# Kernel tuning notes

Hardware: AMD Instinct MI355X
Metric: run time of the kernel (lower is better)

The kernel has to match this reference:

```python
import jax, jax.numpy as jnp
import numpy as np

NUM_HEADS = 12
NUM_PATCHES = 196


def _make_relative_distance_index(num_patches=NUM_PATCHES):
    size = int(np.sqrt(num_patches))  # 14
    coords = np.stack(np.meshgrid(np.arange(size), np.arange(size), indexing='ij'))  # [2,14,14]
    flat = coords.reshape(2, -1)  # [2,196]
    rel = flat[:, None, :] - flat[:, :, None]  # [2,196,196]
    rel = rel.transpose(1, 2, 0).astype(np.int64)  # [196,196,2]
    rel[:, :, 0] += size - 1
    rel[:, :, 1] += size - 1
    rel[:, :, 0] *= 2 * size - 1
    idx = rel.sum(-1) + 1  # shift for cls slot at table row 0
    full = np.zeros((num_patches + 1, num_patches + 1), dtype=np.int64)
    full[1:, 1:] = idx
    return full


def setup_inputs() -> dict:
    key = jax.random.key(0)
    k1, k2, k3, k4, k5 = jax.random.split(key, 5)
    B, N, C = 64, NUM_PATCHES + 1, 768
    table_size = (2 * int(np.sqrt(NUM_PATCHES)) - 1) ** 2 + 1  # 730
    x = jax.random.normal(k1, (B, N, C), dtype=jnp.float32)
    table = jax.random.normal(k2, (table_size, NUM_HEADS), dtype=jnp.float32) * 0.02
    w_qkv = jax.random.normal(k3, (3 * C, C), dtype=jnp.float32) * 0.02
    w_proj = jax.random.normal(k4, (C, C), dtype=jnp.float32) * 0.02
    b_proj = jax.random.normal(k5, (C,), dtype=jnp.float32) * 0.02
    rel_index = jnp.asarray(_make_relative_distance_index())
    return {"x": x, "table": table, "w_qkv": w_qkv, "w_proj": w_proj,
            "b_proj": b_proj, "rel_index": rel_index}


def reference(x, table, w_qkv, w_proj, b_proj, rel_index):
    B, N, C = x.shape
    H = NUM_HEADS
    hd = C // H
    scale = hd ** -0.5
    # qkv projection: [B,N,3C] -> [3,B,H,N,hd]
    qkv = (x @ w_qkv.T).reshape(B, N, 3, H, hd).transpose(2, 0, 3, 1, 4)
    q, k, v = qkv[0], qkv[1], qkv[2]
    # gathered relative position bias: [N,N,H] -> [H,N,N]
    bias = table[rel_index].transpose(2, 0, 1)
    scores = jnp.einsum('bhnd,bhmd->bhnm', q, k) * scale + bias[None]
    attn = jax.nn.softmax(scores, axis=-1)
    out = jnp.einsum('bhnm,bhmd->bhnd', attn, v)
    out = out.transpose(0, 2, 1, 3).reshape(B, N, C)
    return out @ w_proj.T + b_proj
```

## Files before the change

### kernel.cpp

```cpp
#include <hip/hip_runtime.h>


#define NB   64
#define NN   197
#define NC   768
#define NH   12
#define HD   64
#define MM   (NB*NN)
#define MR   12672
#define NP   208
#define VS   212
#define SZQ  ((size_t)NB * NH * NN * HD)
#define CVTQ ((MM + 2304 + 768) * 192)
#define BIASN (NH * 13 * 13 * 256)

typedef unsigned short ushort_t;
typedef __attribute__((ext_vector_type(8))) short short8;
typedef __attribute__((ext_vector_type(4))) float f32x4;
union U128 { uint4 u; short8 s; };

__device__ __forceinline__ unsigned bf16_rne(float f) {
    unsigned u = __float_as_uint(f);
    return (u + 0x7fffu + ((u >> 16) & 1u)) >> 16;
}

__device__ __forceinline__ void gld16(unsigned short* lds, const unsigned short* g) {
    __builtin_amdgcn_global_load_lds(
        (const __attribute__((address_space(1))) void*)g,
        (__attribute__((address_space(3))) void*)lds, 16, 0, 0);
}

__global__ __launch_bounds__(256) void prepare(
    const float* __restrict__ x, const float* __restrict__ w_qkv,
    const float* __restrict__ w_proj, const float* __restrict__ table,
    const int* __restrict__ rel_index,
    ushort_t* __restrict__ xh, ushort_t* __restrict__ wh,
    ushort_t* __restrict__ wp, float* __restrict__ biasP)
{
    int idx = blockIdx.x * 256 + threadIdx.x;
    if (idx < CVTQ) {
        int r = idx / 192;
        int c = (idx - r * 192) * 4;
        const float* src;
        ushort_t* dsth;
        if (r < MM) {
            src = x + (size_t)r * NC; dsth = xh + (size_t)r * NC + c;
        } else if (r < MM + 2304) {
            int rr = r - MM;
            src = w_qkv + (size_t)rr * NC; dsth = wh + (size_t)rr * NC + c;
        } else {
            int rr = r - MM - 2304;
            src = w_proj + (size_t)rr * NC; dsth = wp + (size_t)rr * NC + c;
        }
        float4 f = *(const float4*)(src + c);
        ushort4 hv = { (ushort_t)bf16_rne(f.x), (ushort_t)bf16_rne(f.y),
                       (ushort_t)bf16_rne(f.z), (ushort_t)bf16_rne(f.w) };
        *(ushort4*)dsth = hv;
    } else {
        int i = idx - CVTQ;
        if (i < BIASN) {
            int r = i & 3, l15 = (i >> 2) & 15, quad = (i >> 6) & 3;
            int t = i >> 8;
            int kt = t % 13; int t2 = t / 13;
            int qt = t2 % 13; int h = t2 / 13;
            int n = qt * 16 + quad * 4 + r;
            int m = kt * 16 + l15;
            float v = -1e30f;
            if (n < NN && m < NN) v = table[rel_index[n * NN + m] * NH + h];
            biasP[i] = v;
        }
    }
}

__device__ __forceinline__ void gemm_mainloop(
    const ushort_t* __restrict__ A2, int sA,
    const ushort_t* __restrict__ B2, int sB,
    int m0, int n0, int kiters, ushort_t* Abuf, ushort_t* Bbuf, f32x4 acc[4][8])
{
    const int tid = threadIdx.x;
    const int w = tid >> 6, lane = tid & 63;
    const int wm = w & 1, wn = w >> 1;
    const int lr = lane >> 3, lc = lane & 7;
    const int gch = lc ^ lr;

    const ushort_t* Ag = A2 + (size_t)(m0 + w * 32 + lr) * sA + gch * 8;
    const ushort_t* Bg = B2 + (size_t)(n0 + w * 64 + lr) * sB + gch * 8;
    ushort_t* Al = Abuf + (w * 32) * 64;
    ushort_t* Bl = Bbuf + (w * 64) * 64;

    int aoff[4], boff[8];
    const int quad = lane >> 4, l15 = lane & 15;
    #pragma unroll
    for (int t = 0; t < 4; t++) {
        int ra = wm * 64 + t * 16 + l15;
        aoff[t] = ra * 64 + ((quad ^ (ra & 7)) << 3);
    }
    #pragma unroll
    for (int j = 0; j < 8; j++) {
        int rb = wn * 128 + j * 16 + l15;
        boff[j] = rb * 64 + ((quad ^ (rb & 7)) << 3);
    }

    for (int ks = 0; ks < kiters; ks++) {
        __syncthreads();
        #pragma unroll
        for (int it = 0; it < 4; it++)
            gld16(Al + it * 8 * 64, Ag + (size_t)it * 8 * sA);
        #pragma unroll
        for (int it = 0; it < 8; it++)
            gld16(Bl + it * 8 * 64, Bg + (size_t)it * 8 * sB);
        __syncthreads();
        #pragma unroll
        for (int k0 = 0; k0 < 2; k0++) {
            U128 af[4], bf[8];
            #pragma unroll
            for (int t = 0; t < 4; t++)
                af[t].u = *(const uint4*)&Abuf[aoff[t] ^ (k0 << 5)];
            #pragma unroll
            for (int j = 0; j < 8; j++)
                bf[j].u = *(const uint4*)&Bbuf[boff[j] ^ (k0 << 5)];
            #pragma unroll
            for (int i = 0; i < 4; i++)
                #pragma unroll
                for (int j = 0; j < 8; j++)
                    acc[i][j] = __builtin_amdgcn_mfma_f32_16x16x32_bf16(
                        af[i].s, bf[j].s, acc[i][j], 0, 0, 0);
        }
        Ag += 64; Bg += 64;
    }
}

__device__ __forceinline__ int xcd_remap(int bid, int nwg) {
    int q8 = nwg >> 3, r8 = nwg & 7;
    int xcd = bid & 7, loc = bid >> 3;
    return (xcd < r8 ? xcd * (q8 + 1) : r8 * (q8 + 1) + (xcd - r8) * q8) + loc;
}

__global__ __launch_bounds__(256, 2) void gemm_qkv_mfma(
    const ushort_t* __restrict__ A2, const ushort_t* __restrict__ B2,
    ushort_t* __restrict__ qbf, ushort_t* __restrict__ kbf,
    ushort_t* __restrict__ vbf)
{
    __shared__ ushort_t Abuf[128 * 64];
    __shared__ ushort_t Bbuf[256 * 64];
    f32x4 acc[4][8];
    f32x4 z = {0.f, 0.f, 0.f, 0.f};
    #pragma unroll
    for (int i = 0; i < 4; i++)
        #pragma unroll
        for (int j = 0; j < 8; j++) acc[i][j] = z;

    int f = xcd_remap(blockIdx.x, 891);
    int mt_ = f / 9, nt_ = f - mt_ * 9;
    const int m0 = mt_ * 128, n0 = nt_ * 256;
    gemm_mainloop(A2, NC, B2, NC, m0, n0, 12, Abuf, Bbuf, acc);

    __syncthreads();

    const int tid = threadIdx.x;
    const int w = tid >> 6, lane = tid & 63;
    const int wm = w & 1, wn = w >> 1;
    const int quad = lane >> 4, l15 = lane & 15;

    ushort_t* Sw = Abuf + w * 1152;
    const int orow = lane >> 2;
    const int dch = (lane & 3) << 3;
    #pragma unroll
    for (int mt = 0; mt < 4; mt++) {
        int m = m0 + wm * 64 + mt * 16 + orow;
        int b_ = m / NN, n_ = m - b_ * NN;
        bool mv = (m < MM);
        #pragma unroll
        for (int g = 0; g < 2; g++) {
            int cg = n0 + wn * 128 + g * 64;
            int tq = cg / NC;
            int wi = cg - tq * NC;
            int hh = wi >> 6;
            ushort_t* dst = (tq == 0) ? qbf : (tq == 1) ? kbf : vbf;
            float scale = (tq == 0) ? 0.125f : 1.0f;
            #pragma unroll
            for (int nt = 0; nt < 4; nt++)
                #pragma unroll
                for (int r = 0; r < 4; r++)
                    Sw[(quad * 4 + r) * 72 + nt * 16 + l15] =
                        (ushort_t)bf16_rne(acc[mt][g * 4 + nt][r] * scale);
            if (mv) {
                size_t rb = ((size_t)(b_ * NH + hh) * NN + n_) * HD;
                uint4 v0 = *(const uint4*)&Sw[orow * 72 + dch];
                uint4 v1 = *(const uint4*)&Sw[orow * 72 + dch + 32];
                *(uint4*)&dst[rb + dch] = v0;
                *(uint4*)&dst[rb + dch + 32] = v1;
            }
        }
    }
}

__global__ __launch_bounds__(256, 2) void gemm_proj_mfma(
    const ushort_t* __restrict__ A2, const ushort_t* __restrict__ B2,
    const float* __restrict__ bias, float* __restrict__ out)
{
    __shared__ ushort_t Abuf[128 * 64];
    __shared__ ushort_t Bbuf[256 * 64];
    f32x4 acc[4][8];
    f32x4 z = {0.f, 0.f, 0.f, 0.f};
    #pragma unroll
    for (int i = 0; i < 4; i++)
        #pragma unroll
        for (int j = 0; j < 8; j++) acc[i][j] = z;

    int f = xcd_remap(blockIdx.x, 297);
    int mt_ = f / 3, nt_ = f - mt_ * 3;
    const int m0 = mt_ * 128, n0 = nt_ * 256;
    gemm_mainloop(A2, NC, B2, NC, m0, n0, 12, Abuf, Bbuf, acc);

    const int tid = threadIdx.x;
    const int w = tid >> 6, lane = tid & 63;
    const int wm = w & 1, wn = w >> 1;
    const int quad = lane >> 4, l15 = lane & 15;
    #pragma unroll
    for (int nt = 0; nt < 8; nt++) {
        int col = n0 + wn * 128 + nt * 16 + l15;
        float bi = bias[col];
        #pragma unroll
        for (int mt = 0; mt < 4; mt++) {
            #pragma unroll
            for (int r = 0; r < 4; r++) {
                int m = m0 + wm * 64 + mt * 16 + quad * 4 + r;
                if (m < MM)
                    out[(size_t)m * NC + col] = acc[mt][nt][r] + bi;
            }
        }
    }
}

__global__ __launch_bounds__(256, 2) void attn_mfma(
    const ushort_t* __restrict__ qbf, const ushort_t* __restrict__ kbf,
    const ushort_t* __restrict__ vbf, const float* __restrict__ biasP,
    ushort_t* __restrict__ ab)
{
    __shared__ ushort_t Kl[NP * 64];
    __shared__ ushort_t Vt[64 * VS];
    __shared__ ushort_t Pl[4][16 * VS];

    const int bh = blockIdx.x;
    const int b = bh / NH, h = bh % NH;
    const int tid = threadIdx.x;
    const int w = tid >> 6, lane = tid & 63;
    const int quad = lane >> 4, l15 = lane & 15;
    const size_t base = (size_t)bh * (NN * HD);
    const ushort_t* kg = kbf + base;
    const ushort_t* vg = vbf + base;
    const ushort_t* qg = qbf + base;

    for (int idx = tid; idx < NP * 8; idx += 256) {
        int row = idx >> 3, ch = idx & 7;
        int srow = (row < NN) ? row : (NN - 1);
        uint4 val = *(const uint4*)(kg + (size_t)srow * HD + ch * 8);
        *(uint4*)&Kl[row * 64 + ((ch ^ (row & 7)) << 3)] = val;
    }

    ushort_t* Vstage = &Pl[0][0];
    for (int idx = tid; idx < NP * 8; idx += 256) {
        int row = idx >> 3, ch = idx & 7;
        uint4 val = {0u, 0u, 0u, 0u};
        if (row < NN) val = *(const uint4*)(vg + (size_t)row * HD + ch * 8);
        *(uint4*)&Vstage[row * HD + ch * 8] = val;
    }
    __syncthreads();
    for (int task = tid; task < 64 * 26; task += 256) {
        int d = task & 63, kc = task >> 6;
        ushort_t tmp[8];
        #pragma unroll
        for (int j = 0; j < 8; j++)
            tmp[j] = Vstage[(kc * 8 + j) * HD + d];
        uint4 u;
        u.x = (unsigned)tmp[0] | ((unsigned)tmp[1] << 16);
        u.y = (unsigned)tmp[2] | ((unsigned)tmp[3] << 16);
        u.z = (unsigned)tmp[4] | ((unsigned)tmp[5] << 16);
        u.w = (unsigned)tmp[6] | ((unsigned)tmp[7] << 16);
        *(uint4*)&Vt[d * VS + kc * 8] = u;
    }
    __syncthreads();

    const int ksl = (quad ^ (l15 & 7)) << 3;
    ushort_t* P = Pl[w];

    #pragma unroll
    for (int rep = 0; rep < 2; rep++) {
        const int qtA = w + rep * 8;
        const int qtB = qtA + 4;
        const bool hasB = (qtB <= 12);

        const int q0A = qtA * 16;
        int qrA = q0A + l15; if (qrA > NN - 1) qrA = NN - 1;
        U128 qA0, qA1;
        qA0.u = *(const uint4*)(qg + (size_t)qrA * HD + quad * 8);
        qA1.u = *(const uint4*)(qg + (size_t)qrA * HD + 32 + quad * 8);
        f32x4 SA[13];
        const float* bpA = biasP + ((size_t)(h * 13 + qtA) * 13) * 256 + (quad << 6) + (l15 << 2);
        #pragma unroll
        for (int kt = 0; kt < 13; kt++) {
            float4 bv = *(const float4*)(bpA + kt * 256);
            SA[kt][0] = bv.x; SA[kt][1] = bv.y; SA[kt][2] = bv.z; SA[kt][3] = bv.w;
        }

        const int q0B = qtB * 16;
        U128 qB0, qB1;
        f32x4 SB[13];
        if (hasB) {
            int qrB = q0B + l15; if (qrB > NN - 1) qrB = NN - 1;
            qB0.u = *(const uint4*)(qg + (size_t)qrB * HD + quad * 8);
            qB1.u = *(const uint4*)(qg + (size_t)qrB * HD + 32 + quad * 8);
            const float* bpB = biasP + ((size_t)(h * 13 + qtB) * 13) * 256 + (quad << 6) + (l15 << 2);
            #pragma unroll
            for (int kt = 0; kt < 13; kt++) {
                float4 bv = *(const float4*)(bpB + kt * 256);
                SB[kt][0] = bv.x; SB[kt][1] = bv.y; SB[kt][2] = bv.z; SB[kt][3] = bv.w;
            }
        }

        if (hasB) {
            #pragma unroll
            for (int kt = 0; kt < 13; kt++) {
                int ro = (kt * 16 + l15) * 64 + ksl;
                U128 k0, k1;
                k0.u = *(const uint4*)&Kl[ro];
                k1.u = *(const uint4*)&Kl[ro ^ 32];
                SA[kt] = __builtin_amdgcn_mfma_f32_16x16x32_bf16(qA0.s, k0.s, SA[kt], 0, 0, 0);
                SB[kt] = __builtin_amdgcn_mfma_f32_16x16x32_bf16(qB0.s, k0.s, SB[kt], 0, 0, 0);
                SA[kt] = __builtin_amdgcn_mfma_f32_16x16x32_bf16(qA1.s, k1.s, SA[kt], 0, 0, 0);
                SB[kt] = __builtin_amdgcn_mfma_f32_16x16x32_bf16(qB1.s, k1.s, SB[kt], 0, 0, 0);
            }
        } else {
            #pragma unroll
            for (int kt = 0; kt < 13; kt++) {
                int ro = (kt * 16 + l15) * 64 + ksl;
                U128 k0, k1;
                k0.u = *(const uint4*)&Kl[ro];
                k1.u = *(const uint4*)&Kl[ro ^ 32];
                SA[kt] = __builtin_amdgcn_mfma_f32_16x16x32_bf16(qA0.s, k0.s, SA[kt], 0, 0, 0);
                SA[kt] = __builtin_amdgcn_mfma_f32_16x16x32_bf16(qA1.s, k1.s, SA[kt], 0, 0, 0);
            }
        }

        #pragma unroll
        for (int r = 0; r < 4; r++) {
            float mx = SA[0][r];
            #pragma unroll
            for (int kt = 1; kt < 13; kt++) mx = fmaxf(mx, SA[kt][r]);
            mx = fmaxf(mx, __shfl_xor(mx, 1));
            mx = fmaxf(mx, __shfl_xor(mx, 2));
            mx = fmaxf(mx, __shfl_xor(mx, 4));
            mx = fmaxf(mx, __shfl_xor(mx, 8));
            float sum = 0.f;
            #pragma unroll
            for (int kt = 0; kt < 13; kt++) {
                float e = __expf(SA[kt][r] - mx);
                SA[kt][r] = e;
                sum += e;
            }
            sum += __shfl_xor(sum, 1);
            sum += __shfl_xor(sum, 2);
            sum += __shfl_xor(sum, 4);
            sum += __shfl_xor(sum, 8);
            float inv = 1.0f / sum;
            int prow = quad * 4 + r;
            #pragma unroll
            for (int kt = 0; kt < 13; kt++)
                P[prow * VS + kt * 16 + l15] = (ushort_t)bf16_rne(SA[kt][r] * inv);
        }

        f32x4 OA[4];
        f32x4 z4 = {0.f, 0.f, 0.f, 0.f};
        #pragma unroll
        for (int dt = 0; dt < 4; dt++) OA[dt] = z4;
        #pragma unroll
        for (int ks = 0; ks < 7; ks++) {
            int pc = ks * 32 + quad * 8;
            bool vld = (pc < NP);
            int pcc = vld ? pc : 0;
            U128 pf;
            pf.u = *(const uint4*)&P[l15 * VS + pcc];
            if (!vld) { pf.u.x = 0u; pf.u.y = 0u; pf.u.z = 0u; pf.u.w = 0u; }
            #pragma unroll
            for (int dt = 0; dt < 4; dt++) {
                U128 vf;
                vf.u = *(const uint4*)&Vt[(dt * 16 + l15) * VS + pcc];
                OA[dt] = __builtin_amdgcn_mfma_f32_16x16x32_bf16(pf.s, vf.s, OA[dt], 0, 0, 0);
            }
        }

        f32x4 OB[4];
        if (hasB) {
            #pragma unroll
            for (int r = 0; r < 4; r++) {
                float mx = SB[0][r];
                #pragma unroll
                for (int kt = 1; kt < 13; kt++) mx = fmaxf(mx, SB[kt][r]);
                mx = fmaxf(mx, __shfl_xor(mx, 1));
                mx = fmaxf(mx, __shfl_xor(mx, 2));
                mx = fmaxf(mx, __shfl_xor(mx, 4));
                mx = fmaxf(mx, __shfl_xor(mx, 8));
                float sum = 0.f;
                #pragma unroll
                for (int kt = 0; kt < 13; kt++) {
                    float e = __expf(SB[kt][r] - mx);
                    SB[kt][r] = e;
                    sum += e;
                }
                sum += __shfl_xor(sum, 1);
                sum += __shfl_xor(sum, 2);
                sum += __shfl_xor(sum, 4);
                sum += __shfl_xor(sum, 8);
                float inv = 1.0f / sum;
                int prow = quad * 4 + r;
                #pragma unroll
                for (int kt = 0; kt < 13; kt++)
                    P[prow * VS + kt * 16 + l15] = (ushort_t)bf16_rne(SB[kt][r] * inv);
            }
            #pragma unroll
            for (int dt = 0; dt < 4; dt++) OB[dt] = z4;
            #pragma unroll
            for (int ks = 0; ks < 7; ks++) {
                int pc = ks * 32 + quad * 8;
                bool vld = (pc < NP);
                int pcc = vld ? pc : 0;
                U128 pf;
                pf.u = *(const uint4*)&P[l15 * VS + pcc];
                if (!vld) { pf.u.x = 0u; pf.u.y = 0u; pf.u.z = 0u; pf.u.w = 0u; }
                #pragma unroll
                for (int dt = 0; dt < 4; dt++) {
                    U128 vf;
                    vf.u = *(const uint4*)&Vt[(dt * 16 + l15) * VS + pcc];
                    OB[dt] = __builtin_amdgcn_mfma_f32_16x16x32_bf16(pf.s, vf.s, OB[dt], 0, 0, 0);
                }
            }
        }

        {
            float* Osh = (float*)&Pl[w][0];
            #pragma unroll
            for (int dt = 0; dt < 4; dt++)
                #pragma unroll
                for (int r = 0; r < 4; r++)
                    Osh[(quad * 4 + r) * 68 + dt * 16 + l15] = OA[dt][r];
            int orow = lane >> 2;
            int d0 = (lane & 3) << 4;
            int q = q0A + orow;
            if (q < NN) {
                unsigned hiw[8];
                #pragma unroll
                for (int k4 = 0; k4 < 4; k4++) {
                    float4 f = *(const float4*)&Osh[orow * 68 + d0 + k4 * 4];
                    unsigned h0 = bf16_rne(f.x), h1 = bf16_rne(f.y);
                    unsigned h2 = bf16_rne(f.z), h3 = bf16_rne(f.w);
                    hiw[k4 * 2]     = h0 | (h1 << 16);
                    hiw[k4 * 2 + 1] = h2 | (h3 << 16);
                }
                size_t baseo = ((size_t)b * NN + q) * NC + h * HD + d0;
                uint4 hA = {hiw[0], hiw[1], hiw[2], hiw[3]};
                uint4 hB = {hiw[4], hiw[5], hiw[6], hiw[7]};
                *(uint4*)&ab[baseo] = hA;
                *(uint4*)&ab[baseo + 8] = hB;
            }
        }
        if (hasB) {
            float* Osh = (float*)&Pl[w][0];
            #pragma unroll
            for (int dt = 0; dt < 4; dt++)
                #pragma unroll
                for (int r = 0; r < 4; r++)
                    Osh[(quad * 4 + r) * 68 + dt * 16 + l15] = OB[dt][r];
            int orow = lane >> 2;
            int d0 = (lane & 3) << 4;
            int q = q0B + orow;
            if (q < NN) {
                unsigned hiw[8];
                #pragma unroll
                for (int k4 = 0; k4 < 4; k4++) {
                    float4 f = *(const float4*)&Osh[orow * 68 + d0 + k4 * 4];
                    unsigned h0 = bf16_rne(f.x), h1 = bf16_rne(f.y);
                    unsigned h2 = bf16_rne(f.z), h3 = bf16_rne(f.w);
                    hiw[k4 * 2]     = h0 | (h1 << 16);
                    hiw[k4 * 2 + 1] = h2 | (h3 << 16);
                }
                size_t baseo = ((size_t)b * NN + q) * NC + h * HD + d0;
                uint4 hA = {hiw[0], hiw[1], hiw[2], hiw[3]};
                uint4 hB = {hiw[4], hiw[5], hiw[6], hiw[7]};
                *(uint4*)&ab[baseo] = hA;
                *(uint4*)&ab[baseo + 8] = hB;
            }
        }
    }
}

extern "C" void kernel_launch(void* const* d_in, const int* in_sizes, int n_in,
                              void* d_out, int out_size, void* d_ws, size_t ws_size,
                              hipStream_t stream)
{
    const float* x        = (const float*)d_in[0];
    const float* table    = (const float*)d_in[1];
    const float* w_qkv    = (const float*)d_in[2];
    const float* w_proj   = (const float*)d_in[3];
    const float* b_proj   = (const float*)d_in[4];
    const int*   rel_idx  = (const int*)d_in[5];
    float* out = (float*)d_out;

    ushort_t* xh  = (ushort_t*)d_ws;
    ushort_t* wh  = xh + (size_t)MR * NC;
    ushort_t* wp  = wh + (size_t)2304 * NC;
    ushort_t* ab  = wp + (size_t)768 * NC;
    ushort_t* qbf = ab + (size_t)MR * NC;
    ushort_t* kbf = qbf + SZQ;
    ushort_t* vbf = kbf + SZQ;
    float* biasP  = (float*)(vbf + SZQ);

    const int ptot = CVTQ + BIASN;
    prepare<<<(ptot + 255) / 256, 256, 0, stream>>>(
        x, w_qkv, w_proj, table, rel_idx, xh, wh, wp, biasP);

    gemm_qkv_mfma<<<891, 256, 0, stream>>>(xh, wh, qbf, kbf, vbf);
    attn_mfma<<<768, 256, 0, stream>>>(qbf, kbf, vbf, biasP, ab);
    gemm_proj_mfma<<<297, 256, 0, stream>>>(ab, wp, b_proj, out);
}
```

Baseline: 230.0 us.

## Double-buffer GEMM mainloop with async LDS prefetch and K-step of 32

Rewrites the shared GEMM mainloop used by the QKV and projection kernels to double-buffer LDS. Each iteration now issues direct-to-LDS global loads for the next K-slice before computing on the current one. It halves the K tile to 32 so two stages fit in the same LDS footprint, and uses manual vmcnt waits with raw barriers. The aim is to hide global load latency behind MFMA work, at the cost of twice as many iterations and barriers and a new swizzle pattern that must stay correct.

```diff
diff --git a/kernel.cpp b/kernel.cpp
--- a/kernel.cpp
+++ b/kernel.cpp
@@ -29,6 +29,10 @@
         (const __attribute__((address_space(1))) void*)g,
         (__attribute__((address_space(3))) void*)lds, 16, 0, 0);
 }
+
+#define RAWBAR() do { asm volatile("" ::: "memory"); \
+                      __builtin_amdgcn_s_barrier();  \
+                      asm volatile("" ::: "memory"); } while (0)
 
 __global__ __launch_bounds__(256) void prepare(
     const float* __restrict__ x, const float* __restrict__ w_qkv,
@@ -80,54 +84,63 @@
     const int tid = threadIdx.x;
     const int w = tid >> 6, lane = tid & 63;
     const int wm = w & 1, wn = w >> 1;
-    const int lr = lane >> 3, lc = lane & 7;
-    const int gch = lc ^ lr;
-
-    const ushort_t* Ag = A2 + (size_t)(m0 + w * 32 + lr) * sA + gch * 8;
-    const ushort_t* Bg = B2 + (size_t)(n0 + w * 64 + lr) * sB + gch * 8;
-    ushort_t* Al = Abuf + (w * 32) * 64;
-    ushort_t* Bl = Bbuf + (w * 64) * 64;
-
+    const int quad = lane >> 4, l15 = lane & 15;
+    const int lrow = lane >> 2;
+    const int gch = (lane & 3) ^ ((lane >> 3) & 3);
+
+    const ushort_t* Ag0 = A2 + (size_t)(m0 + w * 32 + lrow) * sA + gch * 8;
+    const ushort_t* Bg0 = B2 + (size_t)(n0 + w * 64 + lrow) * sB + gch * 8;
+
+    ushort_t* Ad0 = Abuf + w * 1024;
+    ushort_t* Bd0 = Bbuf + w * 2048;
+
+#define STAGE(curb, koff) do {                                   \
+    gld16(Ad0 + (curb) * 4096,        Ag0 + (koff));             \
+    gld16(Ad0 + (curb) * 4096 + 512,  Ag0 + (size_t)16 * sA + (koff)); \
+    gld16(Bd0 + (curb) * 8192,        Bg0 + (koff));             \
+    gld16(Bd0 + (curb) * 8192 + 512,  Bg0 + (size_t)16 * sB + (koff)); \
+    gld16(Bd0 + (curb) * 8192 + 1024, Bg0 + (size_t)32 * sB + (koff)); \
+    gld16(Bd0 + (curb) * 8192 + 1536, Bg0 + (size_t)48 * sB + (koff)); \
+} while (0)
+
+    const int rs = (quad ^ ((l15 >> 1) & 3)) << 3;
     int aoff[4], boff[8];
-    const int quad = lane >> 4, l15 = lane & 15;
-    #pragma unroll
-    for (int t = 0; t < 4; t++) {
-        int ra = wm * 64 + t * 16 + l15;
-        aoff[t] = ra * 64 + ((quad ^ (ra & 7)) << 3);
-    }
-    #pragma unroll
-    for (int j = 0; j < 8; j++) {
-        int rb = wn * 128 + j * 16 + l15;
-        boff[j] = rb * 64 + ((quad ^ (rb & 7)) << 3);
-    }
-
-    for (int ks = 0; ks < kiters; ks++) {
-        __syncthreads();
-        #pragma unroll
-        for (int it = 0; it < 4; it++)
-            gld16(Al + it * 8 * 64, Ag + (size_t)it * 8 * sA);
-        #pragma unroll
-        for (int it = 0; it < 8; it++)
-            gld16(Bl + it * 8 * 64, Bg + (size_t)it * 8 * sB);
-        __syncthreads();
-        #pragma unroll
-        for (int k0 = 0; k0 < 2; k0++) {
-            U128 af[4], bf[8];
-            #pragma unroll
-            for (int t = 0; t < 4; t++)
-                af[t].u = *(const uint4*)&Abuf[aoff[t] ^ (k0 << 5)];
+    #pragma unroll
+    for (int i = 0; i < 4; i++)
+        aoff[i] = (wm * 64 + i * 16 + l15) * 32 + rs;
+    #pragma unroll
+    for (int j = 0; j < 8; j++)
+        boff[j] = (wn * 128 + j * 16 + l15) * 32 + rs;
+
+    STAGE(0, 0);
+
+    for (int t = 0; t < kiters; ++t) {
+        const int cur = t & 1;
+        if (t + 1 < kiters) {
+            STAGE(cur ^ 1, (size_t)(t + 1) * 32);
+            asm volatile("s_waitcnt vmcnt(6)" ::: "memory");
+        } else {
+            asm volatile("s_waitcnt vmcnt(0)" ::: "memory");
+        }
+        RAWBAR();
+
+        const ushort_t* Ac = Abuf + cur * 4096;
+        const ushort_t* Bc = Bbuf + cur * 8192;
+        U128 af[4], bf[8];
+        #pragma unroll
+        for (int i = 0; i < 4; i++) af[i].u = *(const uint4*)&Ac[aoff[i]];
+        #pragma unroll
+        for (int j = 0; j < 8; j++) bf[j].u = *(const uint4*)&Bc[boff[j]];
+        #pragma unroll
+        for (int i = 0; i < 4; i++)
             #pragma unroll
             for (int j = 0; j < 8; j++)
-                bf[j].u = *(const uint4*)&Bbuf[boff[j] ^ (k0 << 5)];
-            #pragma unroll
-            for (int i = 0; i < 4; i++)
-                #pragma unroll
-                for (int j = 0; j < 8; j++)
-                    acc[i][j] = __builtin_amdgcn_mfma_f32_16x16x32_bf16(
-                        af[i].s, bf[j].s, acc[i][j], 0, 0, 0);
-        }
-        Ag += 64; Bg += 64;
-    }
+                acc[i][j] = __builtin_amdgcn_mfma_f32_16x16x32_bf16(
+                    af[i].s, bf[j].s, acc[i][j], 0, 0, 0);
+
+        RAWBAR();
+    }
+#undef STAGE
 }
 
 __device__ __forceinline__ int xcd_remap(int bid, int nwg) {
@@ -141,8 +154,8 @@
     ushort_t* __restrict__ qbf, ushort_t* __restrict__ kbf,
     ushort_t* __restrict__ vbf)
 {
-    __shared__ ushort_t Abuf[128 * 64];
-    __shared__ ushort_t Bbuf[256 * 64];
+    __shared__ ushort_t Abuf[2 * 128 * 32];
+    __shared__ ushort_t Bbuf[2 * 256 * 32];
     f32x4 acc[4][8];
     f32x4 z = {0.f, 0.f, 0.f, 0.f};
     #pragma unroll
@@ -153,7 +166,7 @@
     int f = xcd_remap(blockIdx.x, 891);
     int mt_ = f / 9, nt_ = f - mt_ * 9;
     const int m0 = mt_ * 128, n0 = nt_ * 256;
-    gemm_mainloop(A2, NC, B2, NC, m0, n0, 12, Abuf, Bbuf, acc);
+    gemm_mainloop(A2, NC, B2, NC, m0, n0, 24, Abuf, Bbuf, acc);
 
     __syncthreads();
 
@@ -199,8 +212,8 @@
     const ushort_t* __restrict__ A2, const ushort_t* __restrict__ B2,
     const float* __restrict__ bias, float* __restrict__ out)
 {
-    __shared__ ushort_t Abuf[128 * 64];
-    __shared__ ushort_t Bbuf[256 * 64];
+    __shared__ ushort_t Abuf[2 * 128 * 32];
+    __shared__ ushort_t Bbuf[2 * 256 * 32];
     f32x4 acc[4][8];
     f32x4 z = {0.f, 0.f, 0.f, 0.f};
     #pragma unroll
@@ -211,7 +224,7 @@
     int f = xcd_remap(blockIdx.x, 297);
     int mt_ = f / 3, nt_ = f - mt_ * 3;
     const int m0 = mt_ * 128, n0 = nt_ * 256;
-    gemm_mainloop(A2, NC, B2, NC, m0, n0, 12, Abuf, Bbuf, acc);
+    gemm_mainloop(A2, NC, B2, NC, m0, n0, 24, Abuf, Bbuf, acc);
 
     const int tid = threadIdx.x;
     const int w = tid >> 6, lane = tid & 63;
```

Measured after the change: 241.0 us. 4.8% more time.
